# Kernel optimization log

Measured on AMD Instinct MI355X. Metric: run time of the kernel, lower is better.

Reference implementation:

```python
import jax, jax.numpy as jnp
import numpy as np

HEADS = 8
DIM_HEAD = 64
TAU = 0.001        # SoftSort temperature
TEMP = 10.0        # GammaAggregator temperature (EspAttention default temperature=10)
SCALE = DIM_HEAD ** -0.5


def setup_inputs() -> dict:
    key = jax.random.key(0)
    k1, k2, k3, k4 = jax.random.split(key, 4)
    x = jax.random.normal(k1, (4, 128, 512), jnp.float32)
    w_qkv = jax.random.normal(k2, (1536, 512), jnp.float32) * 0.02
    w_out = jax.random.normal(k3, (512, 512), jnp.float32) * 0.02
    b_out = jax.random.normal(k4, (512,), jnp.float32) * 0.02
    return {"x": x, "w_qkv": w_qkv, "w_out": w_out, "b_out": b_out}


def _softsort_p2(scores, tau):
    # scores: [B,H,N,L] -> s: [B,H,L,N]
    s = jnp.swapaxes(scores, -1, -2)
    sorted_s = -jnp.sort(-s, axis=-1)                 # descending sort along N
    # pairwise diff: [B,H,L,N(sorted),N(orig)]
    d = s[..., None, :] - sorted_s[..., :, None]
    return jax.nn.softmax(-(d * d) / tau, axis=-1)    # P_hat [B,H,L,N,N]


def reference(x, w_qkv, w_out, b_out):
    B, N, D = x.shape
    qkv = x @ w_qkv.T                                  # [B,N,3*inner]
    q, k, v = jnp.split(qkv, 3, axis=-1)
    def to_heads(t):
        return jnp.swapaxes(t.reshape(B, N, HEADS, DIM_HEAD), 1, 2)  # [B,H,N,d]
    q, k, v = to_heads(q), to_heads(k), to_heads(v)

    X = q * SCALE
    Y = k * SCALE

    Pu = _softsort_p2(X, TAU)                          # [B,H,L,N,N]
    Pv = _softsort_p2(Y, TAU)                          # [B,H,L,N,N]
    # Gamma = Pu^T @ Pv over the sorted axis
    Gamma = jnp.einsum('bhlki,bhlkj->bhlij', Pu, Pv)   # [B,H,L,N,N]

    # cdist(X, Y, p=2): [B,H,N,N]
    sq = (jnp.sum(X * X, -1)[..., :, None]
          + jnp.sum(Y * Y, -1)[..., None, :]
          - 2.0 * jnp.einsum('bhnd,bhmd->bhnm', X, Y))
    cost = jnp.sqrt(jnp.maximum(sq, 0.0))

    # swds_l = sum_ij cost_ij * Gamma_lij
    swds = jnp.einsum('bhij,bhlij->bhl', cost, Gamma)  # [B,H,L]
    min_s = jnp.min(swds, axis=-1, keepdims=True)
    e = jnp.exp(-TEMP * (swds - min_s))
    weights = e / jnp.sum(e, axis=-1, keepdims=True)   # [B,H,L]

    attn = jnp.einsum('bhl,bhlij->bhij', weights, Gamma)  # [B,H,N,N]

    out = jnp.einsum('bhij,bhjd->bhid', attn, v)       # [B,H,N,d]
    out = jnp.swapaxes(out, 1, 2).reshape(B, N, HEADS * DIM_HEAD)
    out = out @ w_out.T + b_out                        # to_out (dropout=0)
    return out, attn
```

## Files before the change

### kernel.cpp

```cpp
#include <hip/hip_runtime.h>
#include <math.h>

typedef _Float16 f16x8 __attribute__((ext_vector_type(8)));
typedef _Float16 f16x4 __attribute__((ext_vector_type(4)));
typedef float f32x4 __attribute__((ext_vector_type(4)));

#define NSEQ   128
#define DIMH   64
#define NHEAD  8
#define DMODEL 512
#define SCALE  0.125f
#define SPAD   136

#define OFF_X    0
#define OFF_Y    262144
#define OFF_V    524288
#define OFF_COST 786432
#define OFF_SWDS 1310720
#define OFF_W    1312768
#define OFF_OH   1314816
#define OFF_XT   1576960
#define OFF_YT   1839104
#define OFF_ST   2101248
#define OFF_PART 3674112
#define END_ST   3674112
#define END_PART 12062720

#define P1_SMEM  (NSEQ * SPAD * 2 + (768 + 8) * 4)
#define P2_SMEM  (NSEQ * SPAD * 2 + (768 + 64) * 4)
#define PH_SMEM  (2 * NSEQ * SPAD * 2 + (128 * 3 + 512 + 8) * 4)

__device__ __forceinline__ f16x8 cvt8(f32x4 a, f32x4 b) {
  f16x8 h;
  h[0] = (_Float16)a[0]; h[1] = (_Float16)a[1]; h[2] = (_Float16)a[2]; h[3] = (_Float16)a[3];
  h[4] = (_Float16)b[0]; h[5] = (_Float16)b[1]; h[6] = (_Float16)b[2]; h[7] = (_Float16)b[3];
  return h;
}

__global__ __launch_bounds__(256) void k_qkv_f(const float* __restrict__ x,
                                               const float* __restrict__ wq,
                                               float* __restrict__ ws) {
  __shared__ _Float16 Ah[64][72];
  __shared__ _Float16 Bh[64][72];
  const int r0 = blockIdx.x * 64, c0 = blockIdx.y * 64;
  const int t = threadIdx.x, w = t >> 6, lane = t & 63;
  const int srow = t >> 2, sk = (t & 3) << 4;
  f32x4 acc[4] = {};
  for (int kc = 0; kc < 512; kc += 64) {
    __syncthreads();
    {
      const float* ap = &x[(size_t)(r0 + srow) * 512 + kc + sk];
      const float* bp = &wq[(size_t)(c0 + srow) * 512 + kc + sk];
      f32x4 a0 = *(const f32x4*)&ap[0], a1 = *(const f32x4*)&ap[4];
      f32x4 a2 = *(const f32x4*)&ap[8], a3 = *(const f32x4*)&ap[12];
      f32x4 b0 = *(const f32x4*)&bp[0], b1 = *(const f32x4*)&bp[4];
      f32x4 b2 = *(const f32x4*)&bp[8], b3 = *(const f32x4*)&bp[12];
      *(f16x8*)&Ah[srow][sk]     = cvt8(a0, a1);
      *(f16x8*)&Ah[srow][sk + 8] = cvt8(a2, a3);
      *(f16x8*)&Bh[srow][sk]     = cvt8(b0, b1);
      *(f16x8*)&Bh[srow][sk + 8] = cvt8(b2, b3);
    }
    __syncthreads();
#pragma unroll
    for (int k0 = 0; k0 < 64; k0 += 32) {
      f16x8 a = *(const f16x8*)&Ah[(w << 4) + (lane & 15)][k0 + ((lane >> 4) << 3)];
#pragma unroll
      for (int fj = 0; fj < 4; ++fj) {
        f16x8 b = *(const f16x8*)&Bh[(fj << 4) + (lane & 15)][k0 + ((lane >> 4) << 3)];
        acc[fj] = __builtin_amdgcn_mfma_f32_16x16x32_f16(a, b, acc[fj], 0, 0, 0);
      }
    }
  }
  float* X = ws + OFF_X; float* Y = ws + OFF_Y; float* V = ws + OFF_V;
  float* XT = ws + OFF_XT; float* YT = ws + OFF_YT;
  const int rowb = r0 + (w << 4) + ((lane >> 4) << 2);
#pragma unroll
  for (int fj = 0; fj < 4; ++fj) {
    const int c = c0 + (fj << 4) + (lane & 15);
    const int which = c >> 9, cc = c & 511, h = cc >> 6, d = cc & 63;
#pragma unroll
    for (int r = 0; r < 4; ++r) {
      const int rr = rowb + r, bb = rr >> 7, n = rr & 127;
      const int bh = bb * NHEAD + h;
      float val = acc[fj][r];
      size_t dst = ((size_t)bh * NSEQ + n) * DIMH + d;
      size_t dstT = ((size_t)bh * DIMH + d) * NSEQ + n;
      if (which == 0)      { X[dst] = val * SCALE; XT[dstT] = val * SCALE; }
      else if (which == 1) { Y[dst] = val * SCALE; YT[dstT] = val * SCALE; }
      else                 V[dst] = val;
    }
  }
}

__global__ __launch_bounds__(256) void k_qkv(const float* __restrict__ x,
                                             const float* __restrict__ wqkv,
                                             float* __restrict__ ws, int wrT) {
  __shared__ float xs[64][65];
  __shared__ float wsm[64][65];
  const int r0 = blockIdx.x * 64;
  const int c0 = blockIdx.y * 64;
  const int t = threadIdx.x;
  const int tr = (t >> 4) << 2;
  const int tc = (t & 15) << 2;
  float acc[4][4] = {};
  for (int k0 = 0; k0 < 512; k0 += 64) {
    for (int idx = t; idx < 64 * 64; idx += 256) {
      int i = idx >> 6, j = idx & 63;
      xs[i][j]  = x[(size_t)(r0 + i) * 512 + k0 + j];
      wsm[i][j] = wqkv[(size_t)(c0 + i) * 512 + k0 + j];
    }
    __syncthreads();
    for (int kk = 0; kk < 64; ++kk) {
      float a[4], b[4];
#pragma unroll
      for (int u = 0; u < 4; ++u) { a[u] = xs[tr + u][kk]; b[u] = wsm[tc + u][kk]; }
#pragma unroll
      for (int u = 0; u < 4; ++u)
#pragma unroll
        for (int w = 0; w < 4; ++w) acc[u][w] += a[u] * b[w];
    }
    __syncthreads();
  }
  float* X = ws + OFF_X; float* Y = ws + OFF_Y; float* V = ws + OFF_V;
  float* XT = ws + OFF_XT; float* YT = ws + OFF_YT;
#pragma unroll
  for (int u = 0; u < 4; ++u) {
    int r = r0 + tr + u; int b = r >> 7, n = r & 127;
#pragma unroll
    for (int w = 0; w < 4; ++w) {
      int c = c0 + tc + w;
      float val = acc[u][w];
      int which = c >> 9;
      int cc = c & 511;
      int h = cc >> 6, d = cc & 63;
      int bh = b * NHEAD + h;
      size_t dst = ((size_t)bh * NSEQ + n) * DIMH + d;
      size_t dstT = ((size_t)bh * DIMH + d) * NSEQ + n;
      if (which == 0)      { X[dst] = val * SCALE; if (wrT) XT[dstT] = val * SCALE; }
      else if (which == 1) { Y[dst] = val * SCALE; if (wrT) YT[dstT] = val * SCALE; }
      else                 V[dst] = val;
    }
  }
}

__global__ __launch_bounds__(256) void k_cost(float* __restrict__ ws) {
  __shared__ float Ys[128 * 64];
  __shared__ float Xs[16 * 64];
  __shared__ float xx[16], yy[128];
  const int bh = blockIdx.x, g = blockIdx.y;
  const int t = threadIdx.x;
  const float* Xg = ws + OFF_X + (size_t)bh * NSEQ * DIMH + (size_t)g * 16 * DIMH;
  const float* Yg = ws + OFF_Y + (size_t)bh * NSEQ * DIMH;
  for (int c = t; c < 1024; c += 256) Xs[c] = Xg[c];
  for (int c = t; c < 8192; c += 256) Ys[c] = Yg[c];
  __syncthreads();
  if (t < 128) {
    float s = 0;
    const f32x4* y4 = (const f32x4*)&Ys[t * 64];
#pragma unroll
    for (int d = 0; d < 16; ++d) { f32x4 v = y4[d]; s += v[0]*v[0]+v[1]*v[1]+v[2]*v[2]+v[3]*v[3]; }
    yy[t] = s;
  } else if (t < 144) {
    int i = t - 128; float s = 0;
    const f32x4* x4 = (const f32x4*)&Xs[i * 64];
#pragma unroll
    for (int d = 0; d < 16; ++d) { f32x4 v = x4[d]; s += v[0]*v[0]+v[1]*v[1]+v[2]*v[2]+v[3]*v[3]; }
    xx[i] = s;
  }
  __syncthreads();
  const int i = t >> 4, j0 = (t & 15) << 3;
  f32x4 xr[16];
#pragma unroll
  for (int d = 0; d < 16; ++d) xr[d] = ((const f32x4*)&Xs[i * 64])[d];
  const float xxi = xx[i];
  float* C = ws + OFF_COST + (size_t)bh * NSEQ * NSEQ + (size_t)(g * 16 + i) * NSEQ + j0;
  f32x4 o0, o1;
#pragma unroll
  for (int jj = 0; jj < 8; ++jj) {
    const f32x4* y4 = (const f32x4*)&Ys[(j0 + jj) * 64];
    float dot = 0;
#pragma unroll
    for (int d = 0; d < 16; ++d) {
      f32x4 xv = xr[d], yv = y4[d];
      dot += xv[0]*yv[0] + xv[1]*yv[1] + xv[2]*yv[2] + xv[3]*yv[3];
    }
    float sq = xxi + yy[j0 + jj] - 2.f * dot;
    float cv = sqrtf(fmaxf(sq, 0.f));
    if (jj < 4) o0[jj] = cv; else o1[jj - 4] = cv;
  }
  *(f32x4*)&C[0] = o0;
  *(f32x4*)&C[4] = o1;
}

__global__ __launch_bounds__(256) void k_sortden(float* __restrict__ ws) {
  __shared__ float s_lds[128], ss_lds[128], den2[256];
  const int bid = blockIdx.x;
  const int t = threadIdx.x;
  const float* src = ws + ((bid & 1) ? OFF_YT : OFF_XT) + (size_t)(bid >> 1) * NSEQ;
  float* st = ws + OFF_ST + (size_t)bid * 384;
  if (t < 128) s_lds[t] = src[t];
  __syncthreads();
  if (t < 128) {
    const float v = s_lds[t];
    int rank = 0;
#pragma unroll 4
    for (int m = 0; m < NSEQ; m += 4) {
      f32x4 u = *(const f32x4*)&s_lds[m];
#pragma unroll
      for (int j = 0; j < 4; ++j)
        rank += (u[j] > v) || (u[j] == v && (m + j) < t);
    }
    ss_lds[rank] = v;
  }
  __syncthreads();
  {
    const int k = t & 127, half = t >> 7;
    const float sk = ss_lds[k];
    const float* sb = s_lds + (half << 6);
    float sum = 0.f;
#pragma unroll 4
    for (int m = 0; m < 64; m += 4) {
      f32x4 u = *(const f32x4*)&sb[m];
#pragma unroll
      for (int j = 0; j < 4; ++j) {
        float d = u[j] - sk;
        sum += __expf(-1000.f * d * d);
      }
    }
    den2[(half << 7) + k] = sum;
  }
  __syncthreads();
  if (t < 128) {
    st[t]       = s_lds[t];
    st[128 + t] = ss_lds[t];
    st[256 + t] = 1.f / (den2[t] + den2[128 + t]);
  }
}

__device__ __forceinline__ void gen_PT(const float* __restrict__ st,
                                       _Float16* __restrict__ PT, int t) {
  const int i = t >> 2, k0 = (t & 3) << 5;
  const float si = st[i];
  const float* ssp = st + 128 + k0;
  const float* ivp = st + 256 + k0;
#pragma unroll
  for (int kb = 0; kb < 32; kb += 8) {
    f32x4 sv0 = *(const f32x4*)&ssp[kb];
    f32x4 sv1 = *(const f32x4*)&ssp[kb + 4];
    f32x4 iv0 = *(const f32x4*)&ivp[kb];
    f32x4 iv1 = *(const f32x4*)&ivp[kb + 4];
    f16x8 pk;
#pragma unroll
    for (int j = 0; j < 4; ++j) {
      float d0 = si - sv0[j];
      float d1 = si - sv1[j];
      pk[j]     = (_Float16)(__expf(-1000.f * d0 * d0) * iv0[j]);
      pk[j + 4] = (_Float16)(__expf(-1000.f * d1 * d1) * iv1[j]);
    }
    *reinterpret_cast<f16x8*>(&PT[i * SPAD + k0 + kb]) = pk;
  }
}

__device__ __forceinline__ f16x8 gen_Afrag(float si, const float* __restrict__ ss,
                                           const float* __restrict__ iv, int k) {
  f32x4 s0 = *(const f32x4*)&ss[k], s1 = *(const f32x4*)&ss[k + 4];
  f32x4 i0 = *(const f32x4*)&iv[k], i1 = *(const f32x4*)&iv[k + 4];
  f16x8 a;
#pragma unroll
  for (int j = 0; j < 4; ++j) {
    float d0 = si - s0[j];
    float d1 = si - s1[j];
    a[j]     = (_Float16)(__expf(-1000.f * d0 * d0) * i0[j]);
    a[j + 4] = (_Float16)(__expf(-1000.f * d1 * d1) * i1[j]);
  }
  return a;
}

__device__ void build_PT(const float* __restrict__ col, _Float16* __restrict__ PT,
                         float* s_, float* ss_, float* inv_, float* den4, int t) {
  if (t < NSEQ) s_[t] = col[(size_t)t * DIMH];
  __syncthreads();
  if (t < NSEQ) {
    const float v = s_[t];
    int rank = 0;
#pragma unroll 4
    for (int m = 0; m < NSEQ; m += 4) {
      f32x4 u = *(const f32x4*)&s_[m];
#pragma unroll
      for (int j = 0; j < 4; ++j)
        rank += (u[j] > v) || (u[j] == v && (m + j) < t);
    }
    ss_[rank] = v;
  }
  __syncthreads();
  {
    const int k = t & 127, q = t >> 7;
    const float sk = ss_[k];
    const float* sb = s_ + (q << 5);
    float sum = 0.f;
#pragma unroll 4
    for (int m = 0; m < 32; m += 4) {
      f32x4 u = *(const f32x4*)&sb[m];
#pragma unroll
      for (int j = 0; j < 4; ++j) {
        float d = u[j] - sk;
        sum += __expf(-1000.f * d * d);
      }
    }
    den4[(q << 7) + k] = sum;
  }
  __syncthreads();
  if (t < NSEQ)
    inv_[t] = 1.f / (den4[t] + den4[128 + t] + den4[256 + t] + den4[384 + t]);
  __syncthreads();
  {
    const int i = t >> 2, k0 = (t & 3) << 5;
    const float si = s_[i];
#pragma unroll
    for (int kb = 0; kb < 32; kb += 8) {
      f32x4 sv0 = *(const f32x4*)&ss_[k0 + kb];
      f32x4 sv1 = *(const f32x4*)&ss_[k0 + kb + 4];
      f32x4 iv0 = *(const f32x4*)&inv_[k0 + kb];
      f32x4 iv1 = *(const f32x4*)&inv_[k0 + kb + 4];
      f16x8 pk;
#pragma unroll
      for (int j = 0; j < 4; ++j) {
        float d0 = si - sv0[j];
        float d1 = si - sv1[j];
        pk[j]     = (_Float16)(__expf(-1000.f * d0 * d0) * iv0[j]);
        pk[j + 4] = (_Float16)(__expf(-1000.f * d1 * d1) * iv1[j]);
      }
      *reinterpret_cast<f16x8*>(&PT[i * SPAD + k0 + kb]) = pk;
    }
  }
  __syncthreads();
}

__device__ __forceinline__ f16x8 fragPT(const _Float16* PT, int baserow, int k0, int lane) {
  return *reinterpret_cast<const f16x8*>(
      &PT[(baserow + (lane & 15)) * SPAD + k0 + ((lane >> 4) << 3)]);
}

__global__ __launch_bounds__(512, 4) void k_p1(float* __restrict__ ws) {
  extern __shared__ char smem[];
  _Float16* PvT = (_Float16*)smem;
  float* aux = (float*)(PvT + NSEQ * SPAD);
  float* red = aux + 768;
  const int bhl = blockIdx.x, bh = bhl >> 6;
  const int t = threadIdx.x, w = t >> 6, lane = t & 63;
  const float* stg = ws + OFF_ST + (size_t)bhl * 768;
  for (int i = t; i < 768; i += 512) aux[i] = stg[i];
  __syncthreads();
  gen_PT(aux + 384, PvT, t);
  __syncthreads();
  const int r0 = w << 4;
  const float si = aux[r0 + (lane & 15)];
  const float* ssu = aux + 128;
  const float* ivu = aux + 256;
  const int kq = (lane >> 4) << 3;
  f32x4 acc[8];
#pragma unroll
  for (int b = 0; b < 8; ++b) acc[b] = 0;
#pragma unroll
  for (int kc = 0; kc < 4; ++kc) {
    const int k0 = kc << 5;
    f16x8 a = gen_Afrag(si, ssu, ivu, k0 + kq);
#pragma unroll
    for (int fj = 0; fj < 8; ++fj) {
      f16x8 b = fragPT(PvT, fj << 4, k0, lane);
      acc[fj] = __builtin_amdgcn_mfma_f32_16x16x32_f16(a, b, acc[fj], 0, 0, 0);
    }
  }
  const float* C = ws + OFF_COST + (size_t)bh * NSEQ * NSEQ;
  const int cr = r0 + ((lane >> 4) << 2), cc = lane & 15;
  float part = 0.f;
#pragma unroll
  for (int fj = 0; fj < 8; ++fj)
#pragma unroll
    for (int r = 0; r < 4; ++r)
      part += acc[fj][r] * C[(cr + r) * NSEQ + (fj << 4) + cc];
#pragma unroll
  for (int off = 32; off >= 1; off >>= 1) part += __shfl_xor(part, off);
  if (lane == 0) red[w] = part;
  __syncthreads();
  if (t == 0) {
    float s = 0;
#pragma unroll
    for (int i = 0; i < 8; ++i) s += red[i];
    ws[OFF_SWDS + bhl] = s;
  }
}

__global__ __launch_bounds__(512, 4) void k_phase1_fb(float* __restrict__ ws) {
  extern __shared__ char smem[];
  _Float16* PuT = (_Float16*)smem;
  _Float16* PvT = PuT + NSEQ * SPAD;
  float* s_   = (float*)(PvT + NSEQ * SPAD);
  float* ss_  = s_ + 128;
  float* inv_ = ss_ + 128;
  float* den4 = inv_ + 128;
  float* red  = den4 + 512;
  const int bhl = blockIdx.x, bh = bhl >> 6, l = bhl & 63;
  const int t = threadIdx.x, w = t >> 6, lane = t & 63;
  build_PT(ws + OFF_X + (size_t)bh * NSEQ * DIMH + l, PuT, s_, ss_, inv_, den4, t);
  build_PT(ws + OFF_Y + (size_t)bh * NSEQ * DIMH + l, PvT, s_, ss_, inv_, den4, t);
  f32x4 acc[8];
#pragma unroll
  for (int b = 0; b < 8; ++b) acc[b] = 0;
  const int r0 = w << 4;
#pragma unroll
  for (int kc = 0; kc < 4; ++kc) {
    const int k0 = kc << 5;
    f16x8 a0 = fragPT(PuT, r0, k0, lane);
#pragma unroll
    for (int fj = 0; fj < 8; ++fj) {
      f16x8 b = fragPT(PvT, fj << 4, k0, lane);
      acc[fj] = __builtin_amdgcn_mfma_f32_16x16x32_f16(a0, b, acc[fj], 0, 0, 0);
    }
  }
  const float* C = ws + OFF_COST + (size_t)bh * NSEQ * NSEQ;
  const int cr = r0 + ((lane >> 4) << 2), cc = lane & 15;
  float part = 0.f;
#pragma unroll
  for (int fj = 0; fj < 8; ++fj)
#pragma unroll
    for (int r = 0; r < 4; ++r)
      part += acc[fj][r] * C[(cr + r) * NSEQ + (fj << 4) + cc];
#pragma unroll
  for (int off = 32; off >= 1; off >>= 1) part += __shfl_xor(part, off);
  if (lane == 0) red[w] = part;
  __syncthreads();
  if (t == 0) {
    float s = 0;
#pragma unroll
    for (int i = 0; i < 8; ++i) s += red[i];
    ws[OFF_SWDS + bhl] = s;
  }
}

__global__ void k_weights(float* __restrict__ ws) {
  const int bh = blockIdx.x;
  const int l = threadIdx.x;
  float v = ws[OFF_SWDS + bh * 64 + l];
  float mn = v;
#pragma unroll
  for (int off = 32; off >= 1; off >>= 1) mn = fminf(mn, __shfl_xor(mn, off));
  float e = __expf(-10.f * (v - mn));
  float sum = e;
#pragma unroll
  for (int off = 32; off >= 1; off >>= 1) sum += __shfl_xor(sum, off);
  ws[OFF_W + bh * 64 + l] = e / sum;
}

__global__ __launch_bounds__(512, 4) void k_p2w(float* __restrict__ ws) {
  extern __shared__ char smem[];
  _Float16* PvT = (_Float16*)smem;
  float* aux = (float*)(PvT + NSEQ * SPAD);
  float* w_lds = aux + 768;
  const int blk = blockIdx.x, bh = blk >> 4, lc = blk & 15;
  const int t = threadIdx.x, w = t >> 6, lane = t & 63;
  if (t < 64) {
    float v = ws[OFF_SWDS + bh * 64 + t];
    float mn = v;
#pragma unroll
    for (int off = 32; off >= 1; off >>= 1) mn = fminf(mn, __shfl_xor(mn, off));
    float e = __expf(-10.f * (v - mn));
    float sum = e;
#pragma unroll
    for (int off = 32; off >= 1; off >>= 1) sum += __shfl_xor(sum, off);
    w_lds[t] = e / sum;
  }
  __syncthreads();
  const int r0 = w << 4;
  const int kq = (lane >> 4) << 3;
  f32x4 att[8];
#pragma unroll
  for (int b = 0; b < 8; ++b) att[b] = 0;
  for (int q = 0; q < 4; ++q) {
    const int l = (lc << 2) + q;
    const float wl = w_lds[l];
    if (q) __syncthreads();
    const float* stg = ws + OFF_ST + (size_t)(bh * 64 + l) * 768;
    for (int i = t; i < 768; i += 512) aux[i] = stg[i];
    __syncthreads();
    gen_PT(aux + 384, PvT, t);
    __syncthreads();
    const float si = aux[r0 + (lane & 15)];
    const float* ssu = aux + 128;
    const float* ivu = aux + 256;
    f32x4 acc[8];
#pragma unroll
    for (int b = 0; b < 8; ++b) acc[b] = 0;
#pragma unroll
    for (int kc = 0; kc < 4; ++kc) {
      const int k0 = kc << 5;
      f16x8 a = gen_Afrag(si, ssu, ivu, k0 + kq);
#pragma unroll
      for (int fj = 0; fj < 8; ++fj) {
        f16x8 b = fragPT(PvT, fj << 4, k0, lane);
        acc[fj] = __builtin_amdgcn_mfma_f32_16x16x32_f16(a, b, acc[fj], 0, 0, 0);
      }
    }
#pragma unroll
    for (int b = 0; b < 8; ++b) att[b] += wl * acc[b];
  }
  float* P = ws + OFF_PART + (size_t)blk * (NSEQ * NSEQ);
  const int cr = r0 + ((lane >> 4) << 2), cc = lane & 15;
#pragma unroll
  for (int fj = 0; fj < 8; ++fj)
#pragma unroll
    for (int r = 0; r < 4; ++r)
      P[(cr + r) * NSEQ + (fj << 4) + cc] = att[fj][r];
}

__global__ __launch_bounds__(512, 4) void k_phase2_fb(float* __restrict__ ws, float* __restrict__ attn) {
  extern __shared__ char smem[];
  _Float16* PuT = (_Float16*)smem;
  _Float16* PvT = PuT + NSEQ * SPAD;
  float* s_   = (float*)(PvT + NSEQ * SPAD);
  float* ss_  = s_ + 128;
  float* inv_ = ss_ + 128;
  float* den4 = inv_ + 128;
  const int blk = blockIdx.x, bh = blk >> 4, lc = blk & 15;
  const int t = threadIdx.x, w = t >> 6, lane = t & 63;
  const int r0 = w << 4;
  f32x4 att[8];
#pragma unroll
  for (int b = 0; b < 8; ++b) att[b] = 0;
  for (int q = 0; q < 4; ++q) {
    const int l = (lc << 2) + q;
    const float wl = ws[OFF_W + bh * 64 + l];
    build_PT(ws + OFF_X + (size_t)bh * NSEQ * DIMH + l, PuT, s_, ss_, inv_, den4, t);
    build_PT(ws + OFF_Y + (size_t)bh * NSEQ * DIMH + l, PvT, s_, ss_, inv_, den4, t);
    f32x4 acc[8];
#pragma unroll
    for (int b = 0; b < 8; ++b) acc[b] = 0;
#pragma unroll
    for (int kc = 0; kc < 4; ++kc) {
      const int k0 = kc << 5;
      f16x8 a0 = fragPT(PuT, r0, k0, lane);
#pragma unroll
      for (int fj = 0; fj < 8; ++fj) {
        f16x8 b = fragPT(PvT, fj << 4, k0, lane);
        acc[fj] = __builtin_amdgcn_mfma_f32_16x16x32_f16(a0, b, acc[fj], 0, 0, 0);
      }
    }
#pragma unroll
    for (int b = 0; b < 8; ++b) att[b] += wl * acc[b];
  }
  float* A = attn + (size_t)bh * NSEQ * NSEQ;
  const int cr = r0 + ((lane >> 4) << 2), cc = lane & 15;
#pragma unroll
  for (int fj = 0; fj < 8; ++fj)
#pragma unroll
    for (int r = 0; r < 4; ++r)
      atomicAdd(&A[(cr + r) * NSEQ + (fj << 4) + cc], att[fj][r]);
}

__global__ __launch_bounds__(256) void k_avr(float* __restrict__ ws, float* __restrict__ attn) {
  __shared__ float Vs[128 * 64];
  __shared__ float As[16 * 128];
  const int bh = blockIdx.x, g = blockIdx.y;
  const int t = threadIdx.x;
  for (int c = t; c < 2048; c += 256) {
    float s = 0.f;
#pragma unroll
    for (int p = 0; p < 16; ++p)
      s += ws[OFF_PART + ((size_t)(bh * 16 + p)) * 16384 + (size_t)g * 2048 + c];
    As[c] = s;
    attn[(size_t)bh * 16384 + (size_t)g * 2048 + c] = s;
  }
  for (int c = t; c < 8192; c += 256) Vs[c] = ws[OFF_V + (size_t)bh * 8192 + c];
  __syncthreads();
  const int i = t >> 4, dq = t & 15;
  f32x4 acc = {};
  const float* arow = &As[i * 128];
  for (int j = 0; j < 128; ++j) {
    float a = arow[j];
    f32x4 v = ((const f32x4*)&Vs[j * 64])[dq];
    acc += a * v;
  }
  const int b = bh >> 3, h = bh & 7, n = g * 16 + i;
  const size_t obase = ((size_t)(b * NSEQ + n)) * DMODEL + h * DIMH + (dq << 2);
  _Float16* oh16 = (_Float16*)(ws + OFF_XT + 131072) + obase;
  f16x4 hh;
  hh[0] = (_Float16)acc[0]; hh[1] = (_Float16)acc[1];
  hh[2] = (_Float16)acc[2]; hh[3] = (_Float16)acc[3];
  *(f16x4*)oh16 = hh;
}

__global__ __launch_bounds__(256) void k_av(const float* __restrict__ attn, float* __restrict__ ws) {
  __shared__ float Vs[128 * 64];
  __shared__ float As[16 * 128];
  const int bh = blockIdx.x, g = blockIdx.y;
  const int t = threadIdx.x;
  const float* Ag = attn + (size_t)bh * 16384 + (size_t)g * 16 * 128;
  const float* Vg = ws + OFF_V + (size_t)bh * 8192;
  for (int c = t; c < 2048; c += 256) As[c] = Ag[c];
  for (int c = t; c < 8192; c += 256) Vs[c] = Vg[c];
  __syncthreads();
  const int i = t >> 4, dq = t & 15;
  f32x4 acc = {};
  const float* arow = &As[i * 128];
  for (int j = 0; j < 128; ++j) {
    float a = arow[j];
    f32x4 v = ((const f32x4*)&Vs[j * 64])[dq];
    acc += a * v;
  }
  const int b = bh >> 3, h = bh & 7, n = g * 16 + i;
  const size_t obase = ((size_t)(b * NSEQ + n)) * DMODEL + h * DIMH + (dq << 2);
  float* o = ws + OFF_OH + obase;
  *(f32x4*)o = acc;
}

__global__ __launch_bounds__(256) void k_out_f(const float* __restrict__ ws_c,
                                               const float* __restrict__ wout,
                                               const float* __restrict__ bout,
                                               float* __restrict__ out) {
  __shared__ _Float16 Ah[64][72];
  __shared__ _Float16 Bh[64][72];
  const _Float16* ah = (const _Float16*)(ws_c + OFF_XT + 131072);
  const int r0 = blockIdx.x * 64, c0 = blockIdx.y * 64;
  const int t = threadIdx.x, w = t >> 6, lane = t & 63;
  const int srow = t >> 2, sk = (t & 3) << 4;
  f32x4 acc[4] = {};
  for (int kc = 0; kc < 512; kc += 64) {
    __syncthreads();
    {
      *(f16x8*)&Ah[srow][sk]     = *(const f16x8*)&ah[(size_t)(r0 + srow) * 512 + kc + sk];
      *(f16x8*)&Ah[srow][sk + 8] = *(const f16x8*)&ah[(size_t)(r0 + srow) * 512 + kc + sk + 8];
      const float* bp = &wout[(size_t)(c0 + srow) * 512 + kc + sk];
      f32x4 b0 = *(const f32x4*)&bp[0], b1 = *(const f32x4*)&bp[4];
      f32x4 b2 = *(const f32x4*)&bp[8], b3 = *(const f32x4*)&bp[12];
      *(f16x8*)&Bh[srow][sk]     = cvt8(b0, b1);
      *(f16x8*)&Bh[srow][sk + 8] = cvt8(b2, b3);
    }
    __syncthreads();
#pragma unroll
    for (int k0 = 0; k0 < 64; k0 += 32) {
      f16x8 a = *(const f16x8*)&Ah[(w << 4) + (lane & 15)][k0 + ((lane >> 4) << 3)];
#pragma unroll
      for (int fj = 0; fj < 4; ++fj) {
        f16x8 b = *(const f16x8*)&Bh[(fj << 4) + (lane & 15)][k0 + ((lane >> 4) << 3)];
        acc[fj] = __builtin_amdgcn_mfma_f32_16x16x32_f16(a, b, acc[fj], 0, 0, 0);
      }
    }
  }
  const int rowb = r0 + (w << 4) + ((lane >> 4) << 2);
#pragma unroll
  for (int fj = 0; fj < 4; ++fj) {
    const int c = c0 + (fj << 4) + (lane & 15);
    const float bb = bout[c];
#pragma unroll
    for (int r = 0; r < 4; ++r)
      out[(size_t)(rowb + r) * 512 + c] = acc[fj][r] + bb;
  }
}

__global__ __launch_bounds__(256) void k_out(const float* __restrict__ oh,
                                             const float* __restrict__ wout,
                                             const float* __restrict__ bout,
                                             float* __restrict__ out) {
  __shared__ float as_[64][65];
  __shared__ float bs_[64][65];
  const int r0 = blockIdx.x * 64, c0 = blockIdx.y * 64;
  const int t = threadIdx.x;
  const int tr = (t >> 4) << 2, tc = (t & 15) << 2;
  float acc[4][4] = {};
  for (int k0 = 0; k0 < 512; k0 += 64) {
    for (int idx = t; idx < 64 * 64; idx += 256) {
      int i = idx >> 6, j = idx & 63;
      as_[i][j] = oh[(size_t)(r0 + i) * 512 + k0 + j];
      bs_[i][j] = wout[(size_t)(c0 + i) * 512 + k0 + j];
    }
    __syncthreads();
    for (int kk = 0; kk < 64; ++kk) {
      float a[4], b[4];
#pragma unroll
      for (int u = 0; u < 4; ++u) { a[u] = as_[tr + u][kk]; b[u] = bs_[tc + u][kk]; }
#pragma unroll
      for (int u = 0; u < 4; ++u)
#pragma unroll
        for (int w = 0; w < 4; ++w) acc[u][w] += a[u] * b[w];
    }
    __syncthreads();
  }
#pragma unroll
  for (int u = 0; u < 4; ++u)
#pragma unroll
    for (int w = 0; w < 4; ++w)
      out[(size_t)(r0 + tr + u) * 512 + c0 + tc + w] = acc[u][w] + bout[c0 + tc + w];
}

extern "C" void kernel_launch(void* const* d_in, const int* in_sizes, int n_in,
                              void* d_out, int out_size, void* d_ws, size_t ws_size,
                              hipStream_t stream) {
  (void)in_sizes; (void)n_in; (void)out_size;
  const float* x    = (const float*)d_in[0];
  const float* wqkv = (const float*)d_in[1];
  const float* wout = (const float*)d_in[2];
  const float* bout = (const float*)d_in[3];
  float* out  = (float*)d_out;
  float* attn = out + 262144;
  float* ws   = (float*)d_ws;

  const bool fast = ws_size >= (size_t)END_PART * 4;

  if (fast) {
    k_qkv_f<<<dim3(8, 24), 256, 0, stream>>>(x, wqkv, ws);
    k_cost<<<dim3(32, 8), 256, 0, stream>>>(ws);
    k_sortden<<<4096, 256, 0, stream>>>(ws);
    k_p1<<<2048, 512, P1_SMEM, stream>>>(ws);
    k_p2w<<<512, 512, P2_SMEM, stream>>>(ws);
    k_avr<<<dim3(32, 8), 256, 0, stream>>>(ws, attn);
    k_out_f<<<dim3(8, 8), 256, 0, stream>>>(ws, wout, bout, out);
  } else {
    k_qkv<<<dim3(8, 24), 256, 0, stream>>>(x, wqkv, ws, 0);
    k_cost<<<dim3(32, 8), 256, 0, stream>>>(ws);
    k_phase1_fb<<<2048, 512, PH_SMEM, stream>>>(ws);
    k_weights<<<32, 64, 0, stream>>>(ws);
    hipMemsetAsync(attn, 0, 524288 * sizeof(float), stream);
    k_phase2_fb<<<512, 512, PH_SMEM, stream>>>(ws, attn);
    k_av<<<dim3(32, 8), 256, 0, stream>>>(attn, ws);
    k_out<<<dim3(8, 8), 256, 0, stream>>>(ws + OFF_OH, wout, bout, out);
  }
}
```

Before: 131.1 us.

## Fuse Gamma score and weighted accumulation passes via online softmax over L

The separate k_p1 (computing swds per l) and k_p2w (recomputing Gamma to accumulate weighted attention) kernels are merged into one kernel. It uses an online-softmax style running min and normalizer per block of four l values, writes unnormalized partial sums plus (min, Z) pairs, and lets k_avr rescale and normalize the 16 partials. This removes the full second Gamma recomputation (half the MFMA and softsort generation work) and one launch. The cost is that fewer blocks (512 instead of 2048) carry the score pass, with a per-iteration block sync for the reduction.

```diff
diff --git a/kernel.cpp b/kernel.cpp
--- a/kernel.cpp
+++ b/kernel.cpp
@@ -23,11 +23,9 @@
 #define OFF_YT   1839104
 #define OFF_ST   2101248
 #define OFF_PART 3674112
-#define END_ST   3674112
 #define END_PART 12062720
 
-#define P1_SMEM  (NSEQ * SPAD * 2 + (768 + 8) * 4)
-#define P2_SMEM  (NSEQ * SPAD * 2 + (768 + 64) * 4)
+#define PF_SMEM  (NSEQ * SPAD * 2 + (768 + 8) * 4)
 #define PH_SMEM  (2 * NSEQ * SPAD * 2 + (128 * 3 + 512 + 8) * 4)
 
 __device__ __forceinline__ f16x8 cvt8(f32x4 a, f32x4 b) {
@@ -341,53 +339,79 @@
       &PT[(baserow + (lane & 15)) * SPAD + k0 + ((lane >> 4) << 3)]);
 }
 
-__global__ __launch_bounds__(512, 4) void k_p1(float* __restrict__ ws) {
+__global__ __launch_bounds__(512, 4) void k_pf(float* __restrict__ ws) {
   extern __shared__ char smem[];
   _Float16* PvT = (_Float16*)smem;
   float* aux = (float*)(PvT + NSEQ * SPAD);
   float* red = aux + 768;
-  const int bhl = blockIdx.x, bh = bhl >> 6;
+  const int blk = blockIdx.x, bh = blk >> 4, lc = blk & 15;
   const int t = threadIdx.x, w = t >> 6, lane = t & 63;
-  const float* stg = ws + OFF_ST + (size_t)bhl * 768;
-  for (int i = t; i < 768; i += 512) aux[i] = stg[i];
-  __syncthreads();
-  gen_PT(aux + 384, PvT, t);
-  __syncthreads();
   const int r0 = w << 4;
-  const float si = aux[r0 + (lane & 15)];
-  const float* ssu = aux + 128;
-  const float* ivu = aux + 256;
   const int kq = (lane >> 4) << 3;
-  f32x4 acc[8];
-#pragma unroll
-  for (int b = 0; b < 8; ++b) acc[b] = 0;
-#pragma unroll
-  for (int kc = 0; kc < 4; ++kc) {
-    const int k0 = kc << 5;
-    f16x8 a = gen_Afrag(si, ssu, ivu, k0 + kq);
-#pragma unroll
-    for (int fj = 0; fj < 8; ++fj) {
-      f16x8 b = fragPT(PvT, fj << 4, k0, lane);
-      acc[fj] = __builtin_amdgcn_mfma_f32_16x16x32_f16(a, b, acc[fj], 0, 0, 0);
-    }
-  }
   const float* C = ws + OFF_COST + (size_t)bh * NSEQ * NSEQ;
   const int cr = r0 + ((lane >> 4) << 2), cc = lane & 15;
-  float part = 0.f;
+  f32x4 att[8];
+#pragma unroll
+  for (int b = 0; b < 8; ++b) att[b] = 0;
+  float m_run = 3.0e38f, Z = 0.f;
+  for (int q = 0; q < 4; ++q) {
+    const int l = (lc << 2) + q;
+    if (q) __syncthreads();
+    const float* stg = ws + OFF_ST + (size_t)(bh * 64 + l) * 768;
+    for (int i = t; i < 768; i += 512) aux[i] = stg[i];
+    __syncthreads();
+    gen_PT(aux + 384, PvT, t);
+    __syncthreads();
+    const float si = aux[r0 + (lane & 15)];
+    const float* ssu = aux + 128;
+    const float* ivu = aux + 256;
+    f32x4 acc[8];
+#pragma unroll
+    for (int b = 0; b < 8; ++b) acc[b] = 0;
+#pragma unroll
+    for (int kc = 0; kc < 4; ++kc) {
+      const int k0 = kc << 5;
+      f16x8 a = gen_Afrag(si, ssu, ivu, k0 + kq);
+#pragma unroll
+      for (int fj = 0; fj < 8; ++fj) {
+        f16x8 b = fragPT(PvT, fj << 4, k0, lane);
+        acc[fj] = __builtin_amdgcn_mfma_f32_16x16x32_f16(a, b, acc[fj], 0, 0, 0);
+      }
+    }
+    float part = 0.f;
+#pragma unroll
+    for (int fj = 0; fj < 8; ++fj)
+#pragma unroll
+      for (int r = 0; r < 4; ++r)
+        part += acc[fj][r] * C[(cr + r) * NSEQ + (fj << 4) + cc];
+#pragma unroll
+    for (int off = 32; off >= 1; off >>= 1) part += __shfl_xor(part, off);
+    if (lane == 0) red[w] = part;
+    __syncthreads();
+    float swds = ((red[0] + red[1]) + (red[2] + red[3]))
+               + ((red[4] + red[5]) + (red[6] + red[7]));
+    if (swds < m_run) {
+      float sc = __expf(-10.f * (m_run - swds));
+      Z = Z * sc + 1.f;
+#pragma unroll
+      for (int b = 0; b < 8; ++b) att[b] = att[b] * sc + acc[b];
+      m_run = swds;
+    } else {
+      float e = __expf(-10.f * (swds - m_run));
+      Z += e;
+#pragma unroll
+      for (int b = 0; b < 8; ++b) att[b] += e * acc[b];
+    }
+  }
+  float* P = ws + OFF_PART + (size_t)blk * (NSEQ * NSEQ);
 #pragma unroll
   for (int fj = 0; fj < 8; ++fj)
 #pragma unroll
     for (int r = 0; r < 4; ++r)
-      part += acc[fj][r] * C[(cr + r) * NSEQ + (fj << 4) + cc];
-#pragma unroll
-  for (int off = 32; off >= 1; off >>= 1) part += __shfl_xor(part, off);
-  if (lane == 0) red[w] = part;
-  __syncthreads();
+      P[(cr + r) * NSEQ + (fj << 4) + cc] = att[fj][r];
   if (t == 0) {
-    float s = 0;
-#pragma unroll
-    for (int i = 0; i < 8; ++i) s += red[i];
-    ws[OFF_SWDS + bhl] = s;
+    ws[OFF_SWDS + blk * 2]     = m_run;
+    ws[OFF_SWDS + blk * 2 + 1] = Z;
   }
 }
 
@@ -452,67 +476,6 @@
   ws[OFF_W + bh * 64 + l] = e / sum;
 }
 
-__global__ __launch_bounds__(512, 4) void k_p2w(float* __restrict__ ws) {
-  extern __shared__ char smem[];
-  _Float16* PvT = (_Float16*)smem;
-  float* aux = (float*)(PvT + NSEQ * SPAD);
-  float* w_lds = aux + 768;
-  const int blk = blockIdx.x, bh = blk >> 4, lc = blk & 15;
-  const int t = threadIdx.x, w = t >> 6, lane = t & 63;
-  if (t < 64) {
-    float v = ws[OFF_SWDS + bh * 64 + t];
-    float mn = v;
-#pragma unroll
-    for (int off = 32; off >= 1; off >>= 1) mn = fminf(mn, __shfl_xor(mn, off));
-    float e = __expf(-10.f * (v - mn));
-    float sum = e;
-#pragma unroll
-    for (int off = 32; off >= 1; off >>= 1) sum += __shfl_xor(sum, off);
-    w_lds[t] = e / sum;
-  }
-  __syncthreads();
-  const int r0 = w << 4;
-  const int kq = (lane >> 4) << 3;
-  f32x4 att[8];
-#pragma unroll
-  for (int b = 0; b < 8; ++b) att[b] = 0;
-  for (int q = 0; q < 4; ++q) {
-    const int l = (lc << 2) + q;
-    const float wl = w_lds[l];
-    if (q) __syncthreads();
-    const float* stg = ws + OFF_ST + (size_t)(bh * 64 + l) * 768;
-    for (int i = t; i < 768; i += 512) aux[i] = stg[i];
-    __syncthreads();
-    gen_PT(aux + 384, PvT, t);
-    __syncthreads();
-    const float si = aux[r0 + (lane & 15)];
-    const float* ssu = aux + 128;
-    const float* ivu = aux + 256;
-    f32x4 acc[8];
-#pragma unroll
-    for (int b = 0; b < 8; ++b) acc[b] = 0;
-#pragma unroll
-    for (int kc = 0; kc < 4; ++kc) {
-      const int k0 = kc << 5;
-      f16x8 a = gen_Afrag(si, ssu, ivu, k0 + kq);
-#pragma unroll
-      for (int fj = 0; fj < 8; ++fj) {
-        f16x8 b = fragPT(PvT, fj << 4, k0, lane);
-        acc[fj] = __builtin_amdgcn_mfma_f32_16x16x32_f16(a, b, acc[fj], 0, 0, 0);
-      }
-    }
-#pragma unroll
-    for (int b = 0; b < 8; ++b) att[b] += wl * acc[b];
-  }
-  float* P = ws + OFF_PART + (size_t)blk * (NSEQ * NSEQ);
-  const int cr = r0 + ((lane >> 4) << 2), cc = lane & 15;
-#pragma unroll
-  for (int fj = 0; fj < 8; ++fj)
-#pragma unroll
-    for (int r = 0; r < 4; ++r)
-      P[(cr + r) * NSEQ + (fj << 4) + cc] = att[fj][r];
-}
-
 __global__ __launch_bounds__(512, 4) void k_phase2_fb(float* __restrict__ ws, float* __restrict__ attn) {
   extern __shared__ char smem[];
   _Float16* PuT = (_Float16*)smem;
@@ -560,17 +523,39 @@
 __global__ __launch_bounds__(256) void k_avr(float* __restrict__ ws, float* __restrict__ attn) {
   __shared__ float Vs[128 * 64];
   __shared__ float As[16 * 128];
+  __shared__ float F[16];
+  __shared__ float Zinv_s;
   const int bh = blockIdx.x, g = blockIdx.y;
   const int t = threadIdx.x;
+  for (int c = t; c < 8192; c += 256) Vs[c] = ws[OFF_V + (size_t)bh * 8192 + c];
+  if (t == 0) {
+    float mb[16], zb[16], m = 3.0e38f;
+#pragma unroll
+    for (int p = 0; p < 16; ++p) {
+      mb[p] = ws[OFF_SWDS + (bh * 16 + p) * 2];
+      zb[p] = ws[OFF_SWDS + (bh * 16 + p) * 2 + 1];
+      m = fminf(m, mb[p]);
+    }
+    float Zt = 0.f;
+#pragma unroll
+    for (int p = 0; p < 16; ++p) {
+      float f = __expf(-10.f * (mb[p] - m));
+      F[p] = f;
+      Zt += f * zb[p];
+    }
+    Zinv_s = 1.f / Zt;
+  }
+  __syncthreads();
+  const float zi = Zinv_s;
   for (int c = t; c < 2048; c += 256) {
     float s = 0.f;
 #pragma unroll
     for (int p = 0; p < 16; ++p)
-      s += ws[OFF_PART + ((size_t)(bh * 16 + p)) * 16384 + (size_t)g * 2048 + c];
+      s += F[p] * ws[OFF_PART + ((size_t)(bh * 16 + p)) * 16384 + (size_t)g * 2048 + c];
+    s *= zi;
     As[c] = s;
     attn[(size_t)bh * 16384 + (size_t)g * 2048 + c] = s;
   }
-  for (int c = t; c < 8192; c += 256) Vs[c] = ws[OFF_V + (size_t)bh * 8192 + c];
   __syncthreads();
   const int i = t >> 4, dq = t & 15;
   f32x4 acc = {};
@@ -710,8 +695,7 @@
     k_qkv_f<<<dim3(8, 24), 256, 0, stream>>>(x, wqkv, ws);
     k_cost<<<dim3(32, 8), 256, 0, stream>>>(ws);
     k_sortden<<<4096, 256, 0, stream>>>(ws);
-    k_p1<<<2048, 512, P1_SMEM, stream>>>(ws);
-    k_p2w<<<512, 512, P2_SMEM, stream>>>(ws);
+    k_pf<<<512, 512, PF_SMEM, stream>>>(ws);
     k_avr<<<dim3(32, 8), 256, 0, stream>>>(ws, attn);
     k_out_f<<<dim3(8, 8), 256, 0, stream>>>(ws, wout, bout, out);
   } else {
```

After: 134.7 us. 2.7% more time.
